# Kernel optimization log

Hardware: AMD Instinct MI355X
Metric: run time of the kernel (lower is better)

## Reference

```python
import jax, jax.numpy as jnp
import numpy as np

B, S = 4, 1024
VD, TD, HD = 1024, 768, 2048
NH = 16
HDIM = HD // NH
SCALE = HDIM ** -0.5
THRESH = 2.0 / 3.0


def bitnet_linear(x, w, b):
    # BitNet b1.58 eval-mode: per-tensor abs-mean scale, clamp, ternarize, dense matmul
    scale = jnp.clip(jnp.mean(jnp.abs(w)), 1e-5, 1000.0)
    wn = jnp.clip(w / scale, -10.0, 10.0)
    q = jnp.where(wn > THRESH, 1.0, jnp.where(wn < -THRESH, -1.0, 0.0))
    return x @ (q * scale).T + b


def layernorm(x, g, b, eps=1e-5):
    mu = jnp.mean(x, axis=-1, keepdims=True)
    var = jnp.mean(jnp.square(x - mu), axis=-1, keepdims=True)
    return (x - mu) * jax.lax.rsqrt(var + eps) * g + b


def setup_inputs() -> dict:
    key = jax.random.key(0)
    ks = jax.random.split(key, 8)
    return {
        "vision_features": jax.random.normal(ks[0], (B, VD), jnp.float32),
        "text_features": jax.random.normal(ks[1], (B, S, TD), jnp.float32),
        "text_mask": jnp.ones((B, S), dtype=bool),
        "w_vision_proj": jax.random.normal(ks[2], (HD, VD), jnp.float32),
        "b_vision_proj": jnp.zeros((HD,), jnp.float32),
        "w_text_proj": jax.random.normal(ks[3], (HD, TD), jnp.float32),
        "b_text_proj": jnp.zeros((HD,), jnp.float32),
        "w_text_qkv": jax.random.normal(ks[4], (3 * HD, HD), jnp.float32),
        "b_text_qkv": jnp.zeros((3 * HD,), jnp.float32),
        "ln_text_g": jnp.ones((HD,), jnp.float32),
        "ln_text_b": jnp.zeros((HD,), jnp.float32),
        "w_out": jax.random.normal(ks[5], (HD, HD), jnp.float32),
        "b_out": jnp.zeros((HD,), jnp.float32),
        "ln_cross_g": jnp.ones((HD,), jnp.float32),
        "ln_cross_b": jnp.zeros((HD,), jnp.float32),
    }


def reference(vision_features, text_features, text_mask,
              w_vision_proj, b_vision_proj, w_text_proj, b_text_proj,
              w_text_qkv, b_text_qkv, ln_text_g, ln_text_b,
              w_out, b_out, ln_cross_g, ln_cross_b):
    # projections into shared hidden space (BitNet ternary linears)
    vp = bitnet_linear(vision_features, w_vision_proj, b_vision_proj)        # [B, HD]
    tp = bitnet_linear(text_features, w_text_proj, b_text_proj)              # [B, S, HD]

    # --- text self-attention (no rel-pos bias: the rel-pos branch raises and is swallowed) ---
    tn = layernorm(tp, ln_text_g, ln_text_b)
    qkv = bitnet_linear(tn, w_text_qkv, b_text_qkv)                          # [B, S, 3*HD]
    qkv = qkv.reshape(B, S, 3, NH, HDIM).transpose(2, 0, 3, 1, 4)            # [3, B, H, S, hd]
    tq, tk, tv = qkv[0], qkv[1], qkv[2]
    attn = jnp.einsum('bhqd,bhkd->bhqk', tq, tk) * SCALE                     # [B, H, S, S]
    attn = jnp.where(text_mask[:, None, None, :], attn, -1e9)
    attn = jax.nn.softmax(attn, axis=-1)
    text_self = jnp.einsum('bhqk,bhkd->bhqd', attn, tv)
    text_self = text_self.transpose(0, 2, 1, 3).reshape(B, S, HD)
    text_self = tp + text_self                                               # residual (dropout=id in eval)

    # --- image-to-text attention ---
    # original repeats the single vision query over seq then means the (identical)
    # outputs; mathematically equal to a single-query attention.
    vq = vp.reshape(B, NH, 1, HDIM)                                          # [B, H, 1, hd]
    tk2 = text_self.reshape(B, S, NH, HDIM).transpose(0, 2, 1, 3)            # [B, H, S, hd]
    i2t = jnp.einsum('bhqd,bhkd->bhqk', vq, tk2) * SCALE                     # [B, H, 1, S]
    i2t = jnp.where(text_mask[:, None, None, :], i2t, -1e9)
    i2t = jax.nn.softmax(i2t, axis=-1)
    i2t_out = jnp.einsum('bhqk,bhkd->bhqd', i2t, tk2).reshape(B, HD)         # [B, HD]

    # --- text-to-image attention (single kv "token" per head -> softmax over size-1 axis) ---
    tq2 = text_self.reshape(B, S, NH, HDIM).transpose(0, 2, 1, 3)            # [B, H, S, hd]
    vk = vp.reshape(B, NH, 1, HDIM)                                          # [B, H, 1, hd]
    t2i = jnp.einsum('bhqd,bhkd->bhqk', tq2, vk) * SCALE                     # [B, H, S, 1]
    t2i = jax.nn.softmax(t2i, axis=-1)                                       # all ones (size-1 axis)
    t2i_out = jnp.einsum('bhqk,bhkd->bhqd', t2i, vk)                         # [B, H, S, hd]
    t2i_out = t2i_out.transpose(0, 2, 1, 3).reshape(B, S, HD)

    # --- fusion: shared BitNet output projection + cross norm (inferred continuation) ---
    fused_vision = layernorm(vp + bitnet_linear(i2t_out, w_out, b_out), ln_cross_g, ln_cross_b)
    fused_text = layernorm(text_self + bitnet_linear(t2i_out, w_out, b_out), ln_cross_g, ln_cross_b)
    return fused_vision, fused_text
```

## Files before the change

### kernel.cpp

```cpp
#include <hip/hip_runtime.h>


typedef unsigned short u16;
typedef unsigned int   u32;
typedef __attribute__((ext_vector_type(4))) float f32x4;
typedef __attribute__((ext_vector_type(8))) short short8;
typedef _Float16 half8 __attribute__((ext_vector_type(8)));

__device__ __forceinline__ u16 f2h(float x) {
    _Float16 h = (_Float16)x;
    return __builtin_bit_cast(u16, h);
}
__device__ __forceinline__ f32x4 mfmah(short8 a, short8 b, f32x4 c) {
    return __builtin_amdgcn_mfma_f32_16x16x32_f16(
        __builtin_bit_cast(half8, a), __builtin_bit_cast(half8, b), c, 0, 0, 0);
}
__device__ __forceinline__ void gload16(const void* g, void* l) {
    __builtin_amdgcn_global_load_lds((const __attribute__((address_space(1))) u32*)g,
                                     (__attribute__((address_space(3))) u32*)l, 16, 0, 0);
}

__device__ __forceinline__ float blockReduceSum256(float v, float* red) {
#pragma unroll
    for (int o = 32; o; o >>= 1) v += __shfl_down(v, o);
    int lane = threadIdx.x & 63, w = threadIdx.x >> 6;
    __syncthreads();
    if (lane == 0) red[w] = v;
    __syncthreads();
    return red[0] + red[1] + red[2] + red[3];
}

__global__ __launch_bounds__(256) void k_absmean(const float* __restrict__ w, int n4,
                                                 double* __restrict__ part) {
    const float4* w4 = (const float4*)w;
    double s = 0.0;
    for (int i = blockIdx.x * blockDim.x + threadIdx.x; i < n4; i += gridDim.x * blockDim.x) {
        float4 v = w4[i];
        s += (double)fabsf(v.x) + (double)fabsf(v.y) + (double)fabsf(v.z) + (double)fabsf(v.w);
    }
#pragma unroll
    for (int o = 32; o; o >>= 1) s += __shfl_down(s, o);
    __shared__ double p4[4];
    int lane = threadIdx.x & 63, w_ = threadIdx.x >> 6;
    if (lane == 0) p4[w_] = s;
    __syncthreads();
    if (threadIdx.x == 0) part[blockIdx.x] = p4[0] + p4[1] + p4[2] + p4[3];
}

__global__ void k_finalize(const double* __restrict__ part, float* __restrict__ scf) {
    int w = threadIdx.x >> 6, lane = threadIdx.x & 63;
    double s = 0.0;
    for (int j = lane; j < 1024; j += 64) s += part[w * 1024 + j];
#pragma unroll
    for (int o = 32; o; o >>= 1) s += __shfl_down(s, o);
    if (lane == 0) {
        const double ns[4] = {2097152.0, 1572864.0, 12582912.0, 4194304.0};
        float v = (float)(s / ns[w]);
        v = fminf(fmaxf(v, 1e-5f), 1000.0f);
        scf[w] = v;
    }
}

__global__ __launch_bounds__(256) void k_quant(const float* __restrict__ w, u32* __restrict__ qd,
                                               int n2, const float* __restrict__ scf, int slot) {
    float s = scf[slot];
    const float th = 2.0f / 3.0f;
    for (int i = blockIdx.x * blockDim.x + threadIdx.x; i < n2; i += gridDim.x * blockDim.x) {
        float2 v = ((const float2*)w)[i];
        float wn0 = v.x / s, wn1 = v.y / s;
        u32 q0 = (wn0 > th) ? 0x3C00u : ((wn0 < -th) ? 0xBC00u : 0u);
        u32 q1 = (wn1 > th) ? 0x3C00u : ((wn1 < -th) ? 0xBC00u : 0u);
        qd[i] = q0 | (q1 << 16);
    }
}

__global__ __launch_bounds__(256) void k_tofp16(const float* __restrict__ x, u32* __restrict__ xs, int n2) {
    for (int i = blockIdx.x * blockDim.x + threadIdx.x; i < n2; i += gridDim.x * blockDim.x) {
        float2 v = ((const float2*)x)[i];
        xs[i] = (u32)f2h(v.x) | (((u32)f2h(v.y)) << 16);
    }
}

__global__ __launch_bounds__(256) void k_gemm(const u16* __restrict__ A, const u16* __restrict__ Bw,
                                              int K, int N, int NB_N,
                                              const float* __restrict__ scf, int slot,
                                              const float* __restrict__ bias,
                                              float* Cf, u16* Cp, int epi) {
    __shared__ __align__(16) u16 ldsA[128 * 64];
    __shared__ __align__(16) u16 ldsB[128 * 64];
    int m0 = (blockIdx.x / NB_N) * 128;
    int n0 = (blockIdx.x % NB_N) * 128;
    int t = threadIdx.x, lane = t & 63, w = t >> 6;
    int wm = (w >> 1) * 64, wn = (w & 1) * 64;
    f32x4 acc[4][4];
#pragma unroll
    for (int i = 0; i < 4; i++)
#pragma unroll
        for (int j = 0; j < 4; j++) acc[i][j] = (f32x4)(0.0f);

    for (int k0 = 0; k0 < K; k0 += 64) {
        __syncthreads();
#pragma unroll
        for (int i = 0; i < 4; i++) {
            int c = i * 256 + t;
            int row = c & 127, kg = c >> 7;
            const u16* ga = A + (size_t)(m0 + row) * K + (k0 + kg * 8);
            const u16* gb = Bw + (size_t)(n0 + row) * K + (k0 + kg * 8);
            int db = (i * 256 + w * 64) * 8;
            gload16(ga, ldsA + db);
            gload16(gb, ldsB + db);
        }
        __syncthreads();
#pragma unroll
        for (int kk = 0; kk < 64; kk += 32) {
            int kg4 = (kk >> 3) + (lane >> 4);
            short8 av[4], bv[4];
#pragma unroll
            for (int mi = 0; mi < 4; mi++)
                av[mi] = *(const short8*)(ldsA + (size_t)(kg4 * 128 + wm + mi * 16 + (lane & 15)) * 8);
#pragma unroll
            for (int ni = 0; ni < 4; ni++)
                bv[ni] = *(const short8*)(ldsB + (size_t)(kg4 * 128 + wn + ni * 16 + (lane & 15)) * 8);
#pragma unroll
            for (int mi = 0; mi < 4; mi++)
#pragma unroll
                for (int ni = 0; ni < 4; ni++)
                    acc[mi][ni] = mfmah(av[mi], bv[ni], acc[mi][ni]);
        }
    }
    float s = scf[slot];
#pragma unroll
    for (int ni = 0; ni < 4; ni++) {
        int col = n0 + wn + ni * 16 + (lane & 15);
        float bv = bias[col];
#pragma unroll
        for (int mi = 0; mi < 4; mi++) {
            int rb = m0 + wm + mi * 16 + ((lane >> 4) << 2);
#pragma unroll
            for (int j = 0; j < 4; j++) {
                float y = acc[mi][ni][j] * s + bv;
                if (epi == 0) {
                    Cf[(size_t)(rb + j) * N + col] = y;
                } else {
                    Cp[(size_t)(rb + j) * N + col] = f2h(y);
                }
            }
        }
    }
}

__global__ __launch_bounds__(256) void k_vp(const float* __restrict__ vf, const float* __restrict__ w,
                                            const float* __restrict__ bias, const float* __restrict__ scf,
                                            float* __restrict__ vp) {
    __shared__ float xl[4096];
    int t = threadIdx.x;
#pragma unroll
    for (int i = 0; i < 16; i++) xl[t + i * 256] = vf[t + i * 256];
    __syncthreads();
    int lane = t & 63;
    int n = blockIdx.x * 4 + (t >> 6);
    float s = scf[0];
    const float th = 2.0f / 3.0f;
    float a0 = 0, a1 = 0, a2 = 0, a3 = 0;
    const float* wr = w + (size_t)n * 1024;
    for (int k = lane; k < 1024; k += 64) {
        float wn = wr[k] / s;
        float q = (wn > th) ? 1.0f : ((wn < -th) ? -1.0f : 0.0f);
        a0 += xl[k] * q; a1 += xl[1024 + k] * q; a2 += xl[2048 + k] * q; a3 += xl[3072 + k] * q;
    }
#pragma unroll
    for (int o = 32; o; o >>= 1) {
        a0 += __shfl_down(a0, o); a1 += __shfl_down(a1, o);
        a2 += __shfl_down(a2, o); a3 += __shfl_down(a3, o);
    }
    if (lane == 0) {
        float bv = bias[n];
        vp[n] = a0 * s + bv; vp[2048 + n] = a1 * s + bv;
        vp[4096 + n] = a2 * s + bv; vp[6144 + n] = a3 * s + bv;
    }
}

__global__ __launch_bounds__(256) void k_ln1(const float* __restrict__ x, const float* __restrict__ g,
                                             const float* __restrict__ b, u16* __restrict__ tn) {
    __shared__ float red[4];
    int r = blockIdx.x, t = threadIdx.x;
    const float* xr = x + (size_t)r * 2048;
    float v[8]; float s = 0;
#pragma unroll
    for (int i = 0; i < 8; i++) { v[i] = xr[t + i * 256]; s += v[i]; }
    s = blockReduceSum256(s, red);
    float mu = s * (1.0f / 2048.0f);
    float s2 = 0;
#pragma unroll
    for (int i = 0; i < 8; i++) { float d = v[i] - mu; s2 += d * d; }
    s2 = blockReduceSum256(s2, red);
    float rstd = 1.0f / sqrtf(s2 * (1.0f / 2048.0f) + 1e-5f);
#pragma unroll
    for (int i = 0; i < 8; i++) {
        int c = t + i * 256;
        float y = (v[i] - mu) * rstd * g[c] + b[c];
        tn[(size_t)r * 2048 + c] = f2h(y);
    }
}

__global__ __launch_bounds__(256) void k_attn(const u16* __restrict__ qkv, float* ts) {
    __shared__ __align__(16) u16 kp[8192];
    __shared__ __align__(16) u16 vt[128 * 72];
    int t = threadIdx.x, lane = t & 63, w = t >> 6;
    int bh = blockIdx.x >> 4, qb = blockIdx.x & 15;
    int b = bh >> 4, h = bh & 15;
    int rowbase = b * 1024;
    int q0 = qb * 64 + w * 16;
    u16* pl = kp + (size_t)w * 16 * 72;

    short8 qh[4];
    {
        int r = rowbase + q0 + (lane & 15);
        const u16* qp = qkv + (size_t)r * 6144 + h * 128 + (lane >> 4) * 8;
#pragma unroll
        for (int c4 = 0; c4 < 4; c4++) qh[c4] = *(const short8*)(qp + c4 * 32);
    }
    float m[4], ld[4];
#pragma unroll
    for (int j = 0; j < 4; j++) { m[j] = -1e30f; ld[j] = 0.0f; }
    f32x4 po[8];
#pragma unroll
    for (int nt = 0; nt < 8; nt++) po[nt] = (f32x4)(0.0f);
    const float SC = 0.08838834764831845f;

    for (int kt = 0; kt < 16; kt++) {
        __syncthreads();
#pragma unroll
        for (int i = 0; i < 4; i++) {
            int c = i * 256 + t;
            int sl = c & 63, dg = c >> 6;
            const u16* gk = qkv + (size_t)(rowbase + kt * 64 + sl) * 6144 + (2048 + h * 128 + dg * 8);
            gload16(gk, kp + (size_t)(i * 256 + w * 64) * 8);
        }
#pragma unroll
        for (int i = 0; i < 4; i++) {
            int c = i * 256 + t;
            int sl = c & 63, dg = c >> 6;
            const u16* gv = qkv + (size_t)(rowbase + kt * 64 + sl) * 6144 + (4096 + h * 128 + dg * 8);
            short8 vv = *(const short8*)gv;
#pragma unroll
            for (int j = 0; j < 8; j++) vt[(size_t)(dg * 8 + j) * 72 + sl] = (u16)vv[j];
        }
        __syncthreads();

        f32x4 sacc[4];
#pragma unroll
        for (int nt = 0; nt < 4; nt++) sacc[nt] = (f32x4)(0.0f);
#pragma unroll
        for (int c4 = 0; c4 < 4; c4++) {
            int kg = c4 * 4 + (lane >> 4);
#pragma unroll
            for (int nt = 0; nt < 4; nt++) {
                short8 kf = *(const short8*)(kp + (size_t)(kg * 64 + nt * 16 + (lane & 15)) * 8);
                sacc[nt] = mfmah(qh[c4], kf, sacc[nt]);
            }
        }
        float fsc[4], rs[4];
#pragma unroll
        for (int j = 0; j < 4; j++) {
            float mx = fmaxf(fmaxf(sacc[0][j], sacc[1][j]), fmaxf(sacc[2][j], sacc[3][j]));
            mx = fmaxf(mx, __shfl_xor(mx, 1));
            mx = fmaxf(mx, __shfl_xor(mx, 2));
            mx = fmaxf(mx, __shfl_xor(mx, 4));
            mx = fmaxf(mx, __shfl_xor(mx, 8));
            float mn = fmaxf(m[j], mx * SC);
            fsc[j] = expf(m[j] - mn);
            m[j] = mn; rs[j] = 0.0f;
        }
        __syncthreads();
#pragma unroll
        for (int nt = 0; nt < 4; nt++) {
#pragma unroll
            for (int j = 0; j < 4; j++) {
                float p = expf(sacc[nt][j] * SC - m[j]);
                rs[j] += p;
                pl[(size_t)((lane >> 4) * 4 + j) * 72 + nt * 16 + (lane & 15)] = f2h(p);
            }
        }
#pragma unroll
        for (int j = 0; j < 4; j++) {
            float r = rs[j];
            r += __shfl_xor(r, 1); r += __shfl_xor(r, 2);
            r += __shfl_xor(r, 4); r += __shfl_xor(r, 8);
            ld[j] = ld[j] * fsc[j] + r;
        }
#pragma unroll
        for (int nt = 0; nt < 8; nt++)
#pragma unroll
            for (int j = 0; j < 4; j++) po[nt][j] *= fsc[j];

#pragma unroll
        for (int kk2 = 0; kk2 < 2; kk2++) {
            short8 pa = *(const short8*)(pl + (size_t)(lane & 15) * 72 + kk2 * 32 + (lane >> 4) * 8);
#pragma unroll
            for (int nt = 0; nt < 8; nt++) {
                short8 vf = *(const short8*)(vt + (size_t)(nt * 16 + (lane & 15)) * 72 + kk2 * 32 + (lane >> 4) * 8);
                po[nt] = mfmah(pa, vf, po[nt]);
            }
        }
    }
#pragma unroll
    for (int nt = 0; nt < 8; nt++) {
        int d = nt * 16 + (lane & 15);
#pragma unroll
        for (int j = 0; j < 4; j++) {
            int r = rowbase + q0 + (lane >> 4) * 4 + j;
            size_t idx = (size_t)r * 2048 + h * 128 + d;
            ts[idx] = ts[idx] + po[nt][j] / ld[j];
        }
    }
}

__global__ __launch_bounds__(256) void k_i2t(const float* __restrict__ vp, const float* __restrict__ ts,
                                             float* __restrict__ io) {
    __shared__ float vq[128];
    __shared__ float sc[1024];
    __shared__ float red[4];
    __shared__ float part[256];
    int bh = blockIdx.x; int b = bh >> 4, h = bh & 15;
    int t = threadIdx.x, lane = t & 63, w = t >> 6;
    if (t < 128) vq[t] = vp[b * 2048 + h * 128 + t];
    __syncthreads();
    const float SC = 0.08838834764831845f;
    for (int s = w; s < 1024; s += 4) {
        const float* row = ts + (size_t)(b * 1024 + s) * 2048 + h * 128;
        float d = vq[lane] * row[lane] + vq[lane + 64] * row[lane + 64];
#pragma unroll
        for (int o = 32; o; o >>= 1) d += __shfl_down(d, o);
        if (lane == 0) sc[s] = d * SC;
    }
    __syncthreads();
    float mx = -1e30f;
    for (int s = t; s < 1024; s += 256) mx = fmaxf(mx, sc[s]);
#pragma unroll
    for (int o = 32; o; o >>= 1) mx = fmaxf(mx, __shfl_down(mx, o));
    if (lane == 0) red[w] = mx;
    __syncthreads();
    mx = fmaxf(fmaxf(red[0], red[1]), fmaxf(red[2], red[3]));
    __syncthreads();
    float sm = 0;
    for (int s = t; s < 1024; s += 256) { float p = expf(sc[s] - mx); sc[s] = p; sm += p; }
#pragma unroll
    for (int o = 32; o; o >>= 1) sm += __shfl_down(sm, o);
    if (lane == 0) red[w] = sm;
    __syncthreads();
    sm = red[0] + red[1] + red[2] + red[3];
    {
        int d = t & 127, sh = t >> 7;
        float acc = 0;
        const float* base = ts + (size_t)(b * 1024) * 2048 + h * 128 + d;
        for (int s = sh * 512; s < (sh + 1) * 512; s++) acc += sc[s] * base[(size_t)s * 2048];
        part[t] = acc;
    }
    __syncthreads();
    if (t < 128) io[b * 2048 + h * 128 + t] = (part[t] + part[128 + t]) / sm;
}

__global__ __launch_bounds__(256) void k_wout8(const float* __restrict__ i2t, const float* __restrict__ vp,
                                               const float* __restrict__ w, const float* __restrict__ bias,
                                               const float* __restrict__ scf, float* __restrict__ y8) {
    __shared__ float xl[8 * 2048];
    int t = threadIdx.x;
    for (int i = t; i < 16384; i += 256) {
        int rr = i >> 11, cc = i & 2047;
        xl[i] = (rr < 4) ? i2t[rr * 2048 + cc] : vp[(rr - 4) * 2048 + cc];
    }
    __syncthreads();
    int lane = t & 63;
    int n = blockIdx.x * 4 + (t >> 6);
    float s = scf[3];
    const float th = 2.0f / 3.0f;
    float a[8];
#pragma unroll
    for (int i = 0; i < 8; i++) a[i] = 0.0f;
    const float* wr = w + (size_t)n * 2048;
    for (int k = lane; k < 2048; k += 64) {
        float wn = wr[k] / s;
        float q = (wn > th) ? 1.0f : ((wn < -th) ? -1.0f : 0.0f);
#pragma unroll
        for (int i = 0; i < 8; i++) a[i] += xl[i * 2048 + k] * q;
    }
#pragma unroll
    for (int i = 0; i < 8; i++) {
#pragma unroll
        for (int o = 32; o; o >>= 1) a[i] += __shfl_down(a[i], o);
    }
    if (lane == 0) {
        float bv = bias[n];
#pragma unroll
        for (int i = 0; i < 8; i++) y8[i * 2048 + n] = a[i] * s + bv;
    }
}

__global__ __launch_bounds__(256) void k_fln(const float* __restrict__ xa, const float* __restrict__ y8,
                                             const float* __restrict__ g, const float* __restrict__ bb,
                                             float* __restrict__ out, int textmode) {
    __shared__ float red[4];
    int r = blockIdx.x, t = threadIdx.x;
    const float* a = xa + (size_t)r * 2048;
    const float* c = y8 + (size_t)(textmode ? (4 + (r >> 10)) : r) * 2048;
    float v[8]; float s = 0;
#pragma unroll
    for (int i = 0; i < 8; i++) { int cc = t + i * 256; v[i] = a[cc] + c[cc]; s += v[i]; }
    s = blockReduceSum256(s, red);
    float mu = s * (1.0f / 2048.0f);
    float s2 = 0;
#pragma unroll
    for (int i = 0; i < 8; i++) { float d = v[i] - mu; s2 += d * d; }
    s2 = blockReduceSum256(s2, red);
    float rstd = 1.0f / sqrtf(s2 * (1.0f / 2048.0f) + 1e-5f);
#pragma unroll
    for (int i = 0; i < 8; i++) {
        int cc = t + i * 256;
        out[(size_t)r * 2048 + cc] = (v[i] - mu) * rstd * g[cc] + bb[cc];
    }
}

extern "C" void kernel_launch(void* const* d_in, const int* in_sizes, int n_in,
                              void* d_out, int out_size, void* d_ws, size_t ws_size,
                              hipStream_t stream) {
    const float* vf    = (const float*)d_in[0];
    const float* tf    = (const float*)d_in[1];
    const float* w_vp  = (const float*)d_in[3];
    const float* b_vp  = (const float*)d_in[4];
    const float* w_tp  = (const float*)d_in[5];
    const float* b_tp  = (const float*)d_in[6];
    const float* w_qkv = (const float*)d_in[7];
    const float* b_qkv = (const float*)d_in[8];
    const float* lng   = (const float*)d_in[9];
    const float* lnb   = (const float*)d_in[10];
    const float* w_o   = (const float*)d_in[11];
    const float* b_o   = (const float*)d_in[12];
    const float* lcg   = (const float*)d_in[13];
    const float* lcb   = (const float*)d_in[14];
    float* out = (float*)d_out;
    char* ws = (char*)d_ws;

    constexpr size_t OFF_PART  = 0;
    constexpr size_t OFF_SCF   = 49152;
    constexpr size_t OFF_QDTP  = 65536;
    constexpr size_t OFF_QDQKV = 3276800;
    constexpr size_t OFF_XS    = 28442624;
    constexpr size_t OFF_TP    = 34734080;
    constexpr size_t OFF_TN    = 68288512;
    constexpr size_t OFF_QKV   = 85065728;
    constexpr size_t OFF_VP    = 135397376;
    constexpr size_t OFF_I2T   = 135430144;
    constexpr size_t OFF_Y8    = 135462912;

    double* part  = (double*)(ws + OFF_PART);
    float*  scf   = (float*)(ws + OFF_SCF);
    u16*   qd_tp  = (u16*)(ws + OFF_QDTP);
    u16*   qd_qkv = (u16*)(ws + OFF_QDQKV);
    u16*   xs     = (u16*)(ws + OFF_XS);
    float* tpb    = (float*)(ws + OFF_TP);
    u16*   tn     = (u16*)(ws + OFF_TN);
    u16*   qkvp   = (u16*)(ws + OFF_QKV);
    float* vpb    = (float*)(ws + OFF_VP);
    float* i2t    = (float*)(ws + OFF_I2T);
    float* y8     = (float*)(ws + OFF_Y8);

    k_absmean<<<1024, 256, 0, stream>>>(w_vp,  2048 * 1024 / 4, part + 0 * 1024);
    k_absmean<<<1024, 256, 0, stream>>>(w_tp,  2048 * 768  / 4, part + 1 * 1024);
    k_absmean<<<1024, 256, 0, stream>>>(w_qkv, 6144 * 2048 / 4, part + 2 * 1024);
    k_absmean<<<1024, 256, 0, stream>>>(w_o,   2048 * 2048 / 4, part + 3 * 1024);
    k_finalize<<<1, 256, 0, stream>>>(part, scf);

    k_quant<<<2048, 256, 0, stream>>>(w_tp,  (u32*)qd_tp,  2048 * 768  / 2, scf, 1);
    k_quant<<<4096, 256, 0, stream>>>(w_qkv, (u32*)qd_qkv, 6144 * 2048 / 2, scf, 2);
    k_tofp16<<<2048, 256, 0, stream>>>(tf, (u32*)xs, 4096 * 768 / 2);

    k_gemm<<<32 * 16, 256, 0, stream>>>(xs, qd_tp, 768, 2048, 16, scf, 1, b_tp, tpb, nullptr, 0);
    k_vp<<<512, 256, 0, stream>>>(vf, w_vp, b_vp, scf, vpb);

    k_ln1<<<4096, 256, 0, stream>>>(tpb, lng, lnb, tn);

    k_gemm<<<32 * 48, 256, 0, stream>>>(tn, qd_qkv, 2048, 6144, 48, scf, 2, b_qkv, nullptr, qkvp, 1);

    k_attn<<<1024, 256, 0, stream>>>(qkvp, tpb);

    k_i2t<<<64, 256, 0, stream>>>(vpb, tpb, i2t);

    k_wout8<<<512, 256, 0, stream>>>(i2t, vpb, w_o, b_o, scf, y8);

    k_fln<<<4, 256, 0, stream>>>(vpb, y8, lcg, lcb, out, 0);
    k_fln<<<4096, 256, 0, stream>>>(tpb, y8, lcg, lcb, out + 8192, 1);
    (void)in_sizes; (void)n_in; (void)out_size; (void)ws_size;
}
```

Before: 679.9 us.

## Double-buffer GEMM LDS tiles and merge absmean reductions into one launch

```diff
diff --git a/kernel.cpp b/kernel.cpp
--- a/kernel.cpp
+++ b/kernel.cpp
@@ -30,11 +30,16 @@
     return red[0] + red[1] + red[2] + red[3];
 }
 
-__global__ __launch_bounds__(256) void k_absmean(const float* __restrict__ w, int n4,
-                                                 double* __restrict__ part) {
+__global__ __launch_bounds__(256) void k_absmean4(const float* __restrict__ w0, const float* __restrict__ w1,
+                                                  const float* __restrict__ w2, const float* __restrict__ w3,
+                                                  int n40, int n41, int n42, int n43,
+                                                  double* __restrict__ part) {
+    int slot = blockIdx.x >> 8, b = blockIdx.x & 255;
+    const float* w = (slot == 0) ? w0 : (slot == 1) ? w1 : (slot == 2) ? w2 : w3;
+    int n4 = (slot == 0) ? n40 : (slot == 1) ? n41 : (slot == 2) ? n42 : n43;
     const float4* w4 = (const float4*)w;
     double s = 0.0;
-    for (int i = blockIdx.x * blockDim.x + threadIdx.x; i < n4; i += gridDim.x * blockDim.x) {
+    for (int i = b * 256 + threadIdx.x; i < n4; i += 65536) {
         float4 v = w4[i];
         s += (double)fabsf(v.x) + (double)fabsf(v.y) + (double)fabsf(v.z) + (double)fabsf(v.w);
     }
@@ -44,13 +49,13 @@
     int lane = threadIdx.x & 63, w_ = threadIdx.x >> 6;
     if (lane == 0) p4[w_] = s;
     __syncthreads();
-    if (threadIdx.x == 0) part[blockIdx.x] = p4[0] + p4[1] + p4[2] + p4[3];
+    if (threadIdx.x == 0) part[slot * 256 + b] = p4[0] + p4[1] + p4[2] + p4[3];
 }
 
 __global__ void k_finalize(const double* __restrict__ part, float* __restrict__ scf) {
     int w = threadIdx.x >> 6, lane = threadIdx.x & 63;
     double s = 0.0;
-    for (int j = lane; j < 1024; j += 64) s += part[w * 1024 + j];
+    for (int j = lane; j < 256; j += 64) s += part[w * 256 + j];
 #pragma unroll
     for (int o = 32; o; o >>= 1) s += __shfl_down(s, o);
     if (lane == 0) {
@@ -86,8 +91,8 @@
                                               const float* __restrict__ scf, int slot,
                                               const float* __restrict__ bias,
                                               float* Cf, u16* Cp, int epi) {
-    __shared__ __align__(16) u16 ldsA[128 * 64];
-    __shared__ __align__(16) u16 ldsB[128 * 64];
+    __shared__ __align__(16) u16 ldsA[2][128 * 64];
+    __shared__ __align__(16) u16 ldsB[2][128 * 64];
     int m0 = (blockIdx.x / NB_N) * 128;
     int n0 = (blockIdx.x % NB_N) * 128;
     int t = threadIdx.x, lane = t & 63, w = t >> 6;
@@ -98,8 +103,7 @@
 #pragma unroll
         for (int j = 0; j < 4; j++) acc[i][j] = (f32x4)(0.0f);
 
-    for (int k0 = 0; k0 < K; k0 += 64) {
-        __syncthreads();
+    auto STAGE = [&](int buf, int k0) {
 #pragma unroll
         for (int i = 0; i < 4; i++) {
             int c = i * 256 + t;
@@ -107,27 +111,40 @@
             const u16* ga = A + (size_t)(m0 + row) * K + (k0 + kg * 8);
             const u16* gb = Bw + (size_t)(n0 + row) * K + (k0 + kg * 8);
             int db = (i * 256 + w * 64) * 8;
-            gload16(ga, ldsA + db);
-            gload16(gb, ldsB + db);
-        }
-        __syncthreads();
+            gload16(ga, ldsA[buf] + db);
+            gload16(gb, ldsB[buf] + db);
+        }
+    };
+    auto COMPUTE = [&](int buf) {
 #pragma unroll
         for (int kk = 0; kk < 64; kk += 32) {
             int kg4 = (kk >> 3) + (lane >> 4);
             short8 av[4], bv[4];
 #pragma unroll
             for (int mi = 0; mi < 4; mi++)
-                av[mi] = *(const short8*)(ldsA + (size_t)(kg4 * 128 + wm + mi * 16 + (lane & 15)) * 8);
+                av[mi] = *(const short8*)(ldsA[buf] + (size_t)(kg4 * 128 + wm + mi * 16 + (lane & 15)) * 8);
 #pragma unroll
             for (int ni = 0; ni < 4; ni++)
-                bv[ni] = *(const short8*)(ldsB + (size_t)(kg4 * 128 + wn + ni * 16 + (lane & 15)) * 8);
+                bv[ni] = *(const short8*)(ldsB[buf] + (size_t)(kg4 * 128 + wn + ni * 16 + (lane & 15)) * 8);
 #pragma unroll
             for (int mi = 0; mi < 4; mi++)
 #pragma unroll
                 for (int ni = 0; ni < 4; ni++)
                     acc[mi][ni] = mfmah(av[mi], bv[ni], acc[mi][ni]);
         }
-    }
+    };
+
+    STAGE(0, 0);
+    __syncthreads();
+    int cur = 0;
+    for (int k0 = 64; k0 < K; k0 += 64) {
+        STAGE(cur ^ 1, k0);
+        COMPUTE(cur);
+        __syncthreads();
+        cur ^= 1;
+    }
+    COMPUTE(cur);
+
     float s = scf[slot];
 #pragma unroll
     for (int ni = 0; ni < 4; ni++) {
@@ -465,22 +482,21 @@
     float* i2t    = (float*)(ws + OFF_I2T);
     float* y8     = (float*)(ws + OFF_Y8);
 
-    k_absmean<<<1024, 256, 0, stream>>>(w_vp,  2048 * 1024 / 4, part + 0 * 1024);
-    k_absmean<<<1024, 256, 0, stream>>>(w_tp,  2048 * 768  / 4, part + 1 * 1024);
-    k_absmean<<<1024, 256, 0, stream>>>(w_qkv, 6144 * 2048 / 4, part + 2 * 1024);
-    k_absmean<<<1024, 256, 0, stream>>>(w_o,   2048 * 2048 / 4, part + 3 * 1024);
+    k_absmean4<<<1024, 256, 0, stream>>>(w_vp, w_tp, w_qkv, w_o,
+                                         2048 * 1024 / 4, 2048 * 768 / 4,
+                                         6144 * 2048 / 4, 2048 * 2048 / 4, part);
     k_finalize<<<1, 256, 0, stream>>>(part, scf);
 
     k_quant<<<2048, 256, 0, stream>>>(w_tp,  (u32*)qd_tp,  2048 * 768  / 2, scf, 1);
     k_quant<<<4096, 256, 0, stream>>>(w_qkv, (u32*)qd_qkv, 6144 * 2048 / 2, scf, 2);
     k_tofp16<<<2048, 256, 0, stream>>>(tf, (u32*)xs, 4096 * 768 / 2);
 
-    k_gemm<<<32 * 16, 256, 0, stream>>>(xs, qd_tp, 768, 2048, 16, scf, 1, b_tp, tpb, nullptr, 0);
+    k_gemm<<<512, 256, 0, stream>>>(xs, qd_tp, 768, 2048, 16, scf, 1, b_tp, tpb, nullptr, 0);
     k_vp<<<512, 256, 0, stream>>>(vf, w_vp, b_vp, scf, vpb);
 
     k_ln1<<<4096, 256, 0, stream>>>(tpb, lng, lnb, tn);
 
-    k_gemm<<<32 * 48, 256, 0, stream>>>(tn, qd_qkv, 2048, 6144, 48, scf, 2, b_qkv, nullptr, qkvp, 1);
+    k_gemm<<<1536, 256, 0, stream>>>(tn, qd_qkv, 2048, 6144, 48, scf, 2, b_qkv, nullptr, qkvp, 1);
 
     k_attn<<<1024, 256, 0, stream>>>(qkvp, tpb);
 
```

After: 677.3 us. Within noise of the previous version (-0.4%).

## Merge absmean and quant launches; widen QKV GEMM tile to 128x256

Applied to the files above, without the earlier changes.

```diff
diff --git a/kernel.cpp b/kernel.cpp
--- a/kernel.cpp
+++ b/kernel.cpp
@@ -30,11 +30,16 @@
     return red[0] + red[1] + red[2] + red[3];
 }
 
-__global__ __launch_bounds__(256) void k_absmean(const float* __restrict__ w, int n4,
-                                                 double* __restrict__ part) {
+__global__ __launch_bounds__(256) void k_absmean4(const float* __restrict__ w0, const float* __restrict__ w1,
+                                                  const float* __restrict__ w2, const float* __restrict__ w3,
+                                                  int n40, int n41, int n42, int n43,
+                                                  double* __restrict__ part) {
+    int slot = blockIdx.x >> 8, b = blockIdx.x & 255;
+    const float* w = (slot == 0) ? w0 : (slot == 1) ? w1 : (slot == 2) ? w2 : w3;
+    int n4 = (slot == 0) ? n40 : (slot == 1) ? n41 : (slot == 2) ? n42 : n43;
     const float4* w4 = (const float4*)w;
     double s = 0.0;
-    for (int i = blockIdx.x * blockDim.x + threadIdx.x; i < n4; i += gridDim.x * blockDim.x) {
+    for (int i = b * 256 + threadIdx.x; i < n4; i += 65536) {
         float4 v = w4[i];
         s += (double)fabsf(v.x) + (double)fabsf(v.y) + (double)fabsf(v.z) + (double)fabsf(v.w);
     }
@@ -44,13 +49,13 @@
     int lane = threadIdx.x & 63, w_ = threadIdx.x >> 6;
     if (lane == 0) p4[w_] = s;
     __syncthreads();
-    if (threadIdx.x == 0) part[blockIdx.x] = p4[0] + p4[1] + p4[2] + p4[3];
+    if (threadIdx.x == 0) part[slot * 256 + b] = p4[0] + p4[1] + p4[2] + p4[3];
 }
 
 __global__ void k_finalize(const double* __restrict__ part, float* __restrict__ scf) {
     int w = threadIdx.x >> 6, lane = threadIdx.x & 63;
     double s = 0.0;
-    for (int j = lane; j < 1024; j += 64) s += part[w * 1024 + j];
+    for (int j = lane; j < 256; j += 64) s += part[w * 256 + j];
 #pragma unroll
     for (int o = 32; o; o >>= 1) s += __shfl_down(s, o);
     if (lane == 0) {
@@ -61,11 +66,18 @@
     }
 }
 
-__global__ __launch_bounds__(256) void k_quant(const float* __restrict__ w, u32* __restrict__ qd,
-                                               int n2, const float* __restrict__ scf, int slot) {
-    float s = scf[slot];
+__global__ __launch_bounds__(256) void k_quant2(const float* __restrict__ wa, u32* __restrict__ qa, int n2a,
+                                                const float* __restrict__ wb, u32* __restrict__ qb, int n2b,
+                                                const float* __restrict__ scf) {
+    int seg = (blockIdx.x >= 1024) ? 1 : 0;
+    const float* w = seg ? wb : wa;
+    u32* qd = seg ? qb : qa;
+    int n2 = seg ? n2b : n2a;
+    float s = scf[seg ? 2 : 1];
+    int b = seg ? (blockIdx.x - 1024) : blockIdx.x;
+    int nb = seg ? (gridDim.x - 1024) : 1024;
     const float th = 2.0f / 3.0f;
-    for (int i = blockIdx.x * blockDim.x + threadIdx.x; i < n2; i += gridDim.x * blockDim.x) {
+    for (int i = b * 256 + threadIdx.x; i < n2; i += nb * 256) {
         float2 v = ((const float2*)w)[i];
         float wn0 = v.x / s, wn1 = v.y / s;
         u32 q0 = (wn0 > th) ? 0x3C00u : ((wn0 < -th) ? 0xBC00u : 0u);
@@ -144,6 +156,74 @@
                 } else {
                     Cp[(size_t)(rb + j) * N + col] = f2h(y);
                 }
+            }
+        }
+    }
+}
+
+__global__ __launch_bounds__(512, 6) void k_gemm_w(const u16* __restrict__ A, const u16* __restrict__ Bw,
+                                                   int K, int N, int NB_N,
+                                                   const float* __restrict__ scf, int slot,
+                                                   const float* __restrict__ bias,
+                                                   u16* __restrict__ Cp) {
+    __shared__ __align__(16) u16 ldsA[128 * 64];
+    __shared__ __align__(16) u16 ldsB[256 * 64];
+    int m0 = (blockIdx.x / NB_N) * 128;
+    int n0 = (blockIdx.x % NB_N) * 256;
+    int t = threadIdx.x, lane = t & 63, w = t >> 6;
+    int wm = (w & 1) * 64, wn = (w >> 1) * 64;
+    f32x4 acc[4][4];
+#pragma unroll
+    for (int i = 0; i < 4; i++)
+#pragma unroll
+        for (int j = 0; j < 4; j++) acc[i][j] = (f32x4)(0.0f);
+
+    for (int k0 = 0; k0 < K; k0 += 64) {
+        __syncthreads();
+#pragma unroll
+        for (int i = 0; i < 2; i++) {
+            int c = i * 512 + t;
+            int row = c & 127, kg = c >> 7;
+            gload16(A + (size_t)(m0 + row) * K + (k0 + kg * 8),
+                    ldsA + (size_t)(i * 512 + w * 64) * 8);
+        }
+#pragma unroll
+        for (int i = 0; i < 4; i++) {
+            int c = i * 512 + t;
+            int col = c & 255, kg = c >> 8;
+            gload16(Bw + (size_t)(n0 + col) * K + (k0 + kg * 8),
+                    ldsB + (size_t)(i * 512 + w * 64) * 8);
+        }
+        __syncthreads();
+#pragma unroll
+        for (int kk = 0; kk < 64; kk += 32) {
+            int kg4 = (kk >> 3) + (lane >> 4);
+            short8 av[4], bv[4];
+#pragma unroll
+            for (int mi = 0; mi < 4; mi++)
+                av[mi] = *(const short8*)(ldsA + (size_t)(kg4 * 128 + wm + mi * 16 + (lane & 15)) * 8);
+#pragma unroll
+            for (int ni = 0; ni < 4; ni++)
+                bv[ni] = *(const short8*)(ldsB + (size_t)(kg4 * 256 + wn + ni * 16 + (lane & 15)) * 8);
+#pragma unroll
+            for (int mi = 0; mi < 4; mi++)
+#pragma unroll
+                for (int ni = 0; ni < 4; ni++)
+                    acc[mi][ni] = mfmah(av[mi], bv[ni], acc[mi][ni]);
+        }
+    }
+    float s = scf[slot];
+#pragma unroll
+    for (int ni = 0; ni < 4; ni++) {
+        int col = n0 + wn + ni * 16 + (lane & 15);
+        float bv = bias[col];
+#pragma unroll
+        for (int mi = 0; mi < 4; mi++) {
+            int rb = m0 + wm + mi * 16 + ((lane >> 4) << 2);
+#pragma unroll
+            for (int j = 0; j < 4; j++) {
+                float y = acc[mi][ni][j] * s + bv;
+                Cp[(size_t)(rb + j) * N + col] = f2h(y);
             }
         }
     }
@@ -465,22 +545,21 @@
     float* i2t    = (float*)(ws + OFF_I2T);
     float* y8     = (float*)(ws + OFF_Y8);
 
-    k_absmean<<<1024, 256, 0, stream>>>(w_vp,  2048 * 1024 / 4, part + 0 * 1024);
-    k_absmean<<<1024, 256, 0, stream>>>(w_tp,  2048 * 768  / 4, part + 1 * 1024);
-    k_absmean<<<1024, 256, 0, stream>>>(w_qkv, 6144 * 2048 / 4, part + 2 * 1024);
-    k_absmean<<<1024, 256, 0, stream>>>(w_o,   2048 * 2048 / 4, part + 3 * 1024);
+    k_absmean4<<<1024, 256, 0, stream>>>(w_vp, w_tp, w_qkv, w_o,
+                                         2048 * 1024 / 4, 2048 * 768 / 4,
+                                         6144 * 2048 / 4, 2048 * 2048 / 4, part);
     k_finalize<<<1, 256, 0, stream>>>(part, scf);
 
-    k_quant<<<2048, 256, 0, stream>>>(w_tp,  (u32*)qd_tp,  2048 * 768  / 2, scf, 1);
-    k_quant<<<4096, 256, 0, stream>>>(w_qkv, (u32*)qd_qkv, 6144 * 2048 / 2, scf, 2);
+    k_quant2<<<5120, 256, 0, stream>>>(w_tp, (u32*)qd_tp, 2048 * 768 / 2,
+                                       w_qkv, (u32*)qd_qkv, 6144 * 2048 / 2, scf);
     k_tofp16<<<2048, 256, 0, stream>>>(tf, (u32*)xs, 4096 * 768 / 2);
 
-    k_gemm<<<32 * 16, 256, 0, stream>>>(xs, qd_tp, 768, 2048, 16, scf, 1, b_tp, tpb, nullptr, 0);
+    k_gemm<<<512, 256, 0, stream>>>(xs, qd_tp, 768, 2048, 16, scf, 1, b_tp, tpb, nullptr, 0);
     k_vp<<<512, 256, 0, stream>>>(vf, w_vp, b_vp, scf, vpb);
 
     k_ln1<<<4096, 256, 0, stream>>>(tpb, lng, lnb, tn);
 
-    k_gemm<<<32 * 48, 256, 0, stream>>>(tn, qd_qkv, 2048, 6144, 48, scf, 2, b_qkv, nullptr, qkvp, 1);
+    k_gemm_w<<<768, 512, 0, stream>>>(tn, qd_qkv, 2048, 6144, 24, scf, 2, b_qkv, qkvp);
 
     k_attn<<<1024, 256, 0, stream>>>(qkvp, tpb);
 
```

After: 1.045 ms. +53.7%, slower.
